# Kernel tuning notes

Hardware: AMD Instinct MI355X
Metric: run time of the kernel (lower is better)

Reference implementation:

```python
import jax, jax.numpy as jnp
import numpy as np

N, E = 50000, 800000
IN, HID, OUT, H, REL, RD = 768, 256, 128, 8, 6, 64


def setup_inputs() -> dict:
    key = jax.random.key(0)
    ks = jax.random.split(key, 16)
    g = lambda i, shape, sc: jax.random.normal(ks[i], shape, jnp.float32) * sc
    return dict(
        x=g(0, (N, IN), 1.0),
        edge_index=jax.random.randint(ks[1], (2, E), 0, N),
        edge_type=jax.random.randint(ks[2], (E,), 0, REL),
        rel_emb=g(3, (REL, RD), 0.1),
        W1=g(4, (IN, HID), 0.03),
        att_src1=g(5, (H, HID // H), 0.1),
        att_dst1=g(6, (H, HID // H), 0.1),
        We1=g(7, (RD, HID), 0.1),
        att_e1=g(8, (H, HID // H), 0.1),
        b1=jnp.zeros((HID,), jnp.float32),
        g1=jnp.ones((HID,), jnp.float32),
        beta1=jnp.zeros((HID,), jnp.float32),
        W2=g(9, (HID, OUT), 0.06),
        att_src2=g(10, (1, OUT), 0.1),
        att_dst2=g(11, (1, OUT), 0.1),
        b2=jnp.zeros((OUT,), jnp.float32),
        g2=jnp.ones((OUT,), jnp.float32),
        beta2=jnp.zeros((OUT,), jnp.float32),
    )


def _gat(x, src, dst, W, a_s, a_d, bias, heads, ch, e_feat=None, We=None, a_e=None):
    # PyG GATConv (shared lin, concat=True, negative_slope=0.2, eval-mode dropout)
    n = x.shape[0]
    h = (x @ W).reshape(n, heads, ch)              # [N,H,C]
    al_s = (h * a_s).sum(-1)                       # [N,H]
    al_d = (h * a_d).sum(-1)
    alpha = al_s[src] + al_d[dst]                  # [Etot,H]
    if e_feat is not None:
        e = (e_feat @ We).reshape(-1, heads, ch)
        alpha = alpha + (e * a_e).sum(-1)
    alpha = jax.nn.leaky_relu(alpha, 0.2)
    mx = jax.ops.segment_max(alpha, dst, num_segments=n)   # segment softmax over dst
    ex = jnp.exp(alpha - mx[dst])
    den = jax.ops.segment_sum(ex, dst, num_segments=n)
    w = ex / (den[dst] + 1e-16)
    out = jax.ops.segment_sum(h[src] * w[:, :, None], dst, num_segments=n)
    return out.reshape(n, heads * ch) + bias


def _ln(x, g, b):
    m = x.mean(-1, keepdims=True)
    v = x.var(-1, keepdims=True)
    return (x - m) / jnp.sqrt(v + 1e-5) * g + b


def reference(x, edge_index, edge_type, rel_emb, W1, att_src1, att_dst1, We1, att_e1,
              b1, g1, beta1, W2, att_src2, att_dst2, b2, g2, beta2):
    n = x.shape[0]
    src0, dst0 = edge_index[0], edge_index[1]
    loop = jnp.arange(n)
    src = jnp.concatenate([src0, loop])
    dst = jnp.concatenate([dst0, loop])
    rel_feat = rel_emb[edge_type]                   # [E,RD]
    # self-loop edge_attr = mean of incoming edge_attr (fill_value='mean')
    cnt = jax.ops.segment_sum(jnp.ones((src0.shape[0],), jnp.float32), dst0, num_segments=n)
    self_attr = jax.ops.segment_sum(rel_feat, dst0, num_segments=n) / jnp.maximum(cnt, 1.0)[:, None]
    e_feat = jnp.concatenate([rel_feat, self_attr], 0)
    h = _gat(x, src, dst, W1, att_src1, att_dst1, b1, H, HID // H, e_feat, We1, att_e1)
    h = jax.nn.elu(_ln(h, g1, beta1))
    h = _gat(h, src, dst, W2, att_src2, att_dst2, b2, 1, OUT)
    return _ln(h, g2, beta2)
```

## Files before the change

### kernel.cpp

```cpp
#include <hip/hip_runtime.h>
#include <hip/hip_bf16.h>

#define IN_DIM 768
#define HID 256
#define OUT_DIM 128
#define NHEAD 8
#define NREL 6
#define RD 64

typedef unsigned short ushort_t;
typedef float f32x4 __attribute__((ext_vector_type(4)));
typedef __bf16 bf16x8 __attribute__((ext_vector_type(8)));
typedef unsigned short u16x8 __attribute__((ext_vector_type(8)));
typedef unsigned short u16x4 __attribute__((ext_vector_type(4)));
typedef unsigned short u16x2 __attribute__((ext_vector_type(2)));

typedef const __attribute__((address_space(1))) void* gptr_t;
typedef __attribute__((address_space(3))) void* lptr_t;

static __device__ __forceinline__ float leaky(float x) { return x > 0.f ? x : 0.2f * x; }

static __device__ __forceinline__ ushort_t f2bf(float f) {
    union { __hip_bfloat16 h; ushort_t u; } c;
    c.h = __float2bfloat16(f);
    return c.u;
}

static __device__ __forceinline__ float b2f(ushort_t u) {
    union { unsigned int i; float f; } c;
    c.i = ((unsigned int)u) << 16;
    return c.f;
}

__global__ void count_kernel(const int* __restrict__ dst0, int* __restrict__ deg, int E) {
    int e = blockIdx.x * blockDim.x + threadIdx.x;
    if (e >= E) return;
    atomicAdd(&deg[dst0[e]], 1);
}

__global__ void __launch_bounds__(256) scanA(const int* __restrict__ deg,
                                             int* __restrict__ bsum, int n) {
    __shared__ int sh[4];
    int b = blockIdx.x, t = threadIdx.x;
    int s = 0;
#pragma unroll
    for (int j = 0; j < 4; j++) {
        int idx = b * 1024 + t * 4 + j;
        if (idx < n) s += deg[idx];
    }
    for (int o = 32; o > 0; o >>= 1) s += __shfl_xor(s, o, 64);
    if ((t & 63) == 0) sh[t >> 6] = s;
    __syncthreads();
    if (t == 0) bsum[b] = sh[0] + sh[1] + sh[2] + sh[3];
}

__global__ void __launch_bounds__(256) scanB(const int* __restrict__ bsum,
                                             int* __restrict__ bbase,
                                             int* __restrict__ rowptr, int nb, int n) {
    __shared__ int sh[256];
    int t = threadIdx.x;
    int v = (t < nb) ? bsum[t] : 0;
    sh[t] = v;
    __syncthreads();
    for (int o = 1; o < 256; o <<= 1) {
        int add = (t >= o) ? sh[t - o] : 0;
        __syncthreads();
        sh[t] += add;
        __syncthreads();
    }
    if (t < nb) bbase[t] = sh[t] - v;
    if (t == 255) rowptr[n] = sh[255];
}

__global__ void __launch_bounds__(256) scanC(const int* __restrict__ deg,
                                             const int* __restrict__ bbase,
                                             int* __restrict__ rowptr, int n) {
    __shared__ int sh[256];
    int b = blockIdx.x, t = threadIdx.x;
    int base = b * 1024;
    int loc[4];
    int run = 0;
#pragma unroll
    for (int j = 0; j < 4; j++) {
        int idx = base + t * 4 + j;
        int d = (idx < n) ? deg[idx] : 0;
        loc[j] = run;
        run += d;
    }
    int tot = run;
    sh[t] = run;
    __syncthreads();
    for (int o = 1; o < 256; o <<= 1) {
        int add = (t >= o) ? sh[t - o] : 0;
        __syncthreads();
        sh[t] += add;
        __syncthreads();
    }
    int texcl = sh[t] - tot;
    int bb = bbase[b];
#pragma unroll
    for (int j = 0; j < 4; j++) {
        int idx = base + t * 4 + j;
        if (idx < n) rowptr[idx] = bb + texcl + loc[j];
    }
}

__global__ void scatter_kernel(const int* __restrict__ src0, const int* __restrict__ dst0,
                               const int* __restrict__ ety, const int* __restrict__ rowptr,
                               int* __restrict__ fill, int* __restrict__ src_pk, int E) {
    int e = blockIdx.x * blockDim.x + threadIdx.x;
    if (e >= E) return;
    int d = dst0[e];
    int pos = rowptr[d] + atomicAdd(&fill[d], 1);
    src_pk[pos] = src0[e] | (ety[e] << 24);
}

__global__ void rel_alpha_kernel(const float* __restrict__ rel_emb, const float* __restrict__ We1,
                                 const float* __restrict__ att_e1, float* __restrict__ rel_alpha) {
    int t = threadIdx.x;
    if (t >= NREL * NHEAD) return;
    int r = t / NHEAD, h = t % NHEAD;
    float acc = 0.f;
    for (int c = 0; c < HID / NHEAD; c++) {
        float v = 0.f;
        for (int k = 0; k < RD; k++) v += rel_emb[r * RD + k] * We1[k * HID + h * 32 + c];
        acc += v * att_e1[h * 32 + c];
    }
    rel_alpha[r * NHEAD + h] = acc;
}

__global__ void transpose_conv(const float* __restrict__ W, ushort_t* __restrict__ Wt,
                               int K, int Nc) {
    int i = blockIdx.x * 256 + threadIdx.x;
    if (i >= K * Nc) return;
    int k = i / Nc, n = i % Nc;
    Wt[n * K + k] = f2bf(W[i]);
}

__global__ void __launch_bounds__(256) conv_bf16(const float* __restrict__ x,
                                                 ushort_t* __restrict__ xb,
                                                 int total, int padtotal) {
    for (long long idx = (long long)(blockIdx.x * 256 + threadIdx.x) * 8; idx < padtotal;
         idx += (long long)gridDim.x * 256 * 8) {
        u16x8 o;
        if (idx < total) {
            float4 f0 = *reinterpret_cast<const float4*>(x + idx);
            float4 f1 = *reinterpret_cast<const float4*>(x + idx + 4);
            o[0] = f2bf(f0.x); o[1] = f2bf(f0.y); o[2] = f2bf(f0.z); o[3] = f2bf(f0.w);
            o[4] = f2bf(f1.x); o[5] = f2bf(f1.y); o[6] = f2bf(f1.z); o[7] = f2bf(f1.w);
        } else {
            o = u16x8{0, 0, 0, 0, 0, 0, 0, 0};
        }
        *reinterpret_cast<u16x8*>(xb + idx) = o;
    }
}

template <int AMODE>
__global__ void __launch_bounds__(256) gemm_lds(const ushort_t* __restrict__ A,
                                                const ushort_t* __restrict__ Bt,
                                                ushort_t* __restrict__ C,
                                                int K, int Nout, int NBlk,
                                                const float* __restrict__ att_s,
                                                const float* __restrict__ att_d,
                                                float* __restrict__ als,
                                                float* __restrict__ ald, int N) {
    __shared__ ushort_t sA[128 * 64];
    __shared__ ushort_t sB[128 * 64];
    int T = gridDim.x;
    int p = blockIdx.x;
    int q8 = T >> 3, rr8 = T & 7, xc = p & 7, j = p >> 3;
    int l = (xc < rr8 ? xc * (q8 + 1) : rr8 * (q8 + 1) + (xc - rr8) * q8) + j;
    int m0 = (l / NBlk) * 128;
    int n0 = (l % NBlk) * 128;
    int t = threadIdx.x;
    int w = t >> 6, ln = t & 63;
    int wm = (w >> 1) * 64, wn = (w & 1) * 64;

    const ushort_t* ag = A + (size_t)(m0 + w * 32 + (ln >> 3)) * K + (ln & 7) * 8;
    const ushort_t* bg = Bt + (size_t)(n0 + w * 32 + (ln >> 3)) * K + (ln & 7) * 8;

    f32x4 acc[4][4] = {};

    for (int k0 = 0; k0 < K; k0 += 64) {
#pragma unroll
        for (int i = 0; i < 4; i++) {
            __builtin_amdgcn_global_load_lds(
                (gptr_t)(const void*)(ag + (size_t)i * 8 * K + k0),
                (lptr_t)(void*)(&sA[(w * 32 + i * 8) * 64]), 16, 0, 0);
            __builtin_amdgcn_global_load_lds(
                (gptr_t)(const void*)(bg + (size_t)i * 8 * K + k0),
                (lptr_t)(void*)(&sB[(w * 32 + i * 8) * 64]), 16, 0, 0);
        }
        __syncthreads();
#pragma unroll
        for (int ks = 0; ks < 2; ks++) {
            bf16x8 af[4], bfr[4];
#pragma unroll
            for (int m = 0; m < 4; m++)
                af[m] = *reinterpret_cast<const bf16x8*>(
                    &sA[(wm + m * 16 + (ln & 15)) * 64 + ks * 32 + (ln >> 4) * 8]);
#pragma unroll
            for (int n = 0; n < 4; n++)
                bfr[n] = *reinterpret_cast<const bf16x8*>(
                    &sB[(wn + n * 16 + (ln & 15)) * 64 + ks * 32 + (ln >> 4) * 8]);
#pragma unroll
            for (int m = 0; m < 4; m++)
#pragma unroll
                for (int n = 0; n < 4; n++)
                    acc[m][n] = __builtin_amdgcn_mfma_f32_16x16x32_bf16(af[m], bfr[n], acc[m][n], 0, 0, 0);
        }
        __syncthreads();
    }

    int cc = ln & 15, qq = ln >> 4;
#pragma unroll
    for (int m = 0; m < 4; m++) {
#pragma unroll
        for (int rr = 0; rr < 4; rr++) {
            int row = m0 + wm + m * 16 + qq * 4 + rr;
#pragma unroll
            for (int n = 0; n < 4; n++)
                C[(size_t)row * Nout + n0 + wn + n * 16 + cc] = f2bf(acc[m][n][rr]);
        }
    }

    float as_[4], ad_[4];
#pragma unroll
    for (int n = 0; n < 4; n++) {
        int col = n0 + wn + n * 16 + cc;
        as_[n] = att_s[col];
        ad_[n] = att_d[col];
    }

    if constexpr (AMODE == 1) {
        int hbase = (n0 + wn) >> 5;
#pragma unroll
        for (int m = 0; m < 4; m++) {
#pragma unroll
            for (int rr = 0; rr < 4; rr++) {
                int row = m0 + wm + m * 16 + qq * 4 + rr;
                float ps0 = acc[m][0][rr] * as_[0] + acc[m][1][rr] * as_[1];
                float ps1 = acc[m][2][rr] * as_[2] + acc[m][3][rr] * as_[3];
                float pd0 = acc[m][0][rr] * ad_[0] + acc[m][1][rr] * ad_[1];
                float pd1 = acc[m][2][rr] * ad_[2] + acc[m][3][rr] * ad_[3];
#pragma unroll
                for (int o = 1; o < 16; o <<= 1) {
                    ps0 += __shfl_xor(ps0, o, 64);
                    ps1 += __shfl_xor(ps1, o, 64);
                    pd0 += __shfl_xor(pd0, o, 64);
                    pd1 += __shfl_xor(pd1, o, 64);
                }
                if (cc == 0 && row < N) {
                    als[row * NHEAD + hbase] = ps0;
                    als[row * NHEAD + hbase + 1] = ps1;
                    ald[row * NHEAD + hbase] = pd0;
                    ald[row * NHEAD + hbase + 1] = pd1;
                }
            }
        }
    } else {
        __shared__ float sh_s[2][128];
        __shared__ float sh_d[2][128];
#pragma unroll
        for (int m = 0; m < 4; m++) {
#pragma unroll
            for (int rr = 0; rr < 4; rr++) {
                int rib = wm + m * 16 + qq * 4 + rr;
                float ps = acc[m][0][rr] * as_[0] + acc[m][1][rr] * as_[1] +
                           acc[m][2][rr] * as_[2] + acc[m][3][rr] * as_[3];
                float pd = acc[m][0][rr] * ad_[0] + acc[m][1][rr] * ad_[1] +
                           acc[m][2][rr] * ad_[2] + acc[m][3][rr] * ad_[3];
#pragma unroll
                for (int o = 1; o < 16; o <<= 1) {
                    ps += __shfl_xor(ps, o, 64);
                    pd += __shfl_xor(pd, o, 64);
                }
                if (cc == 0) {
                    sh_s[wn >> 6][rib] = ps;
                    sh_d[wn >> 6][rib] = pd;
                }
            }
        }
        __syncthreads();
        if (t < 128) {
            int row = m0 + t;
            if (row < N) {
                als[row] = sh_s[0][t] + sh_s[1][t];
                ald[row] = sh_d[0][t] + sh_d[1][t];
            }
        }
    }
}

__global__ void __launch_bounds__(64) node_agg1(
    const ushort_t* __restrict__ h1b, const float* __restrict__ als, const float* __restrict__ ald,
    const float* __restrict__ rel_alpha, const int* __restrict__ rowptr,
    const int* __restrict__ src_pk,
    const float* __restrict__ b1, const float* __restrict__ g1, const float* __restrict__ beta1,
    ushort_t* __restrict__ out, int N) {
    __shared__ float sh_rel[NREL * NHEAD];
    __shared__ float sh_w[64 * NHEAD];
    __shared__ unsigned sh_off[64];
    int l = threadIdx.x;
    int i = blockIdx.x;
    if (i >= N) return;
    if (l < NREL * NHEAD) sh_rel[l] = rel_alpha[l];
    int h = l & 7;
    int e8 = l >> 3;
    float als_i = als[i * NHEAD + h];
    float ald_h = ald[i * NHEAD + h];
    float c0, c1, c2, c3;
    {
        u16x4 v = *reinterpret_cast<const u16x4*>(h1b + (size_t)i * HID + 4 * l);
        c0 = b2f(v[0]); c1 = b2f(v[1]); c2 = b2f(v[2]); c3 = b2f(v[3]);
    }
    int base = rowptr[i];
    int deg = rowptr[i + 1] - base;
    const char* hb = reinterpret_cast<const char*>(h1b);
    float acc0 = 0.f, acc1 = 0.f, acc2 = 0.f, acc3 = 0.f;
    float csum = 0.f, rs = 0.f;
    __syncthreads();
    for (int cs = 0; cs < deg; cs += 64) {
        int c = min(64, deg - cs);
        for (int p = 0; p * 8 < c; p++) {
            int e = p * 8 + e8;
            if (e < c) {
                int pk = src_pk[base + cs + e];
                int sv = pk & 0xFFFFFF;
                int tv = (unsigned)pk >> 24;
                float ra = sh_rel[tv * NHEAD + h];
                float a = als[sv * NHEAD + h] + ald_h + ra;
                float w = __expf(fminf(leaky(a), 40.f));
                sh_w[e * NHEAD + h] = w;
                csum += w;
                rs += ra;
                if (h == 0) sh_off[e] = (unsigned)sv * (HID * 2);
            }
        }
        __syncthreads();
        int e = 0;
        for (; e + 8 <= c; e += 8) {
            unsigned ofs[8];
            float wt[8];
            u16x4 v[8];
#pragma unroll
            for (int jj = 0; jj < 8; jj++) {
                ofs[jj] = sh_off[e + jj];
                wt[jj] = sh_w[(e + jj) * NHEAD + e8];
            }
#pragma unroll
            for (int jj = 0; jj < 8; jj++)
                v[jj] = *reinterpret_cast<const u16x4*>(hb + ofs[jj] + 8 * l);
#pragma unroll
            for (int jj = 0; jj < 8; jj++) {
                acc0 += wt[jj] * b2f(v[jj][0]);
                acc1 += wt[jj] * b2f(v[jj][1]);
                acc2 += wt[jj] * b2f(v[jj][2]);
                acc3 += wt[jj] * b2f(v[jj][3]);
            }
        }
        for (; e < c; e++) {
            unsigned o0 = sh_off[e];
            float w0 = sh_w[e * NHEAD + e8];
            u16x4 v0 = *reinterpret_cast<const u16x4*>(hb + o0 + 8 * l);
            acc0 += w0 * b2f(v0[0]); acc1 += w0 * b2f(v0[1]);
            acc2 += w0 * b2f(v0[2]); acc3 += w0 * b2f(v0[3]);
        }
        __syncthreads();
    }
    for (int o = 8; o < 64; o <<= 1) {
        csum += __shfl_xor(csum, o, 64);
        rs += __shfl_xor(rs, o, 64);
    }
    float selfa = rs / fmaxf((float)deg, 1.0f);
    float wself = __expf(fminf(leaky(als_i + ald_h + selfa), 40.f));
    float stot = csum + wself;
    float s_g = __shfl(stot, e8, 64);
    float w_g = __shfl(wself, e8, 64);
    acc0 += w_g * c0; acc1 += w_g * c1; acc2 += w_g * c2; acc3 += w_g * c3;
    float inv = 1.0f / (s_g + 1e-16f);
    float4 bb = *reinterpret_cast<const float4*>(b1 + 4 * l);
    float y0 = acc0 * inv + bb.x, y1 = acc1 * inv + bb.y;
    float y2 = acc2 * inv + bb.z, y3 = acc3 * inv + bb.w;
    float su = y0 + y1 + y2 + y3;
    float sq = y0 * y0 + y1 * y1 + y2 * y2 + y3 * y3;
    for (int o = 1; o < 64; o <<= 1) {
        su += __shfl_xor(su, o, 64);
        sq += __shfl_xor(sq, o, 64);
    }
    float mean = su * (1.f / 256.f);
    float var = sq * (1.f / 256.f) - mean * mean;
    float rstd = rsqrtf(var + 1e-5f);
    float4 gg = *reinterpret_cast<const float4*>(g1 + 4 * l);
    float4 be = *reinterpret_cast<const float4*>(beta1 + 4 * l);
    float z0 = (y0 - mean) * rstd * gg.x + be.x;
    float z1 = (y1 - mean) * rstd * gg.y + be.y;
    float z2 = (y2 - mean) * rstd * gg.z + be.z;
    float z3 = (y3 - mean) * rstd * gg.w + be.w;
    u16x4 ov;
    ov[0] = f2bf(z0 > 0.f ? z0 : __expf(z0) - 1.f);
    ov[1] = f2bf(z1 > 0.f ? z1 : __expf(z1) - 1.f);
    ov[2] = f2bf(z2 > 0.f ? z2 : __expf(z2) - 1.f);
    ov[3] = f2bf(z3 > 0.f ? z3 : __expf(z3) - 1.f);
    *reinterpret_cast<u16x4*>(out + (size_t)i * HID + 4 * l) = ov;
}

__global__ void __launch_bounds__(64) node_agg2(const ushort_t* __restrict__ h2b,
                                                const float* __restrict__ als,
                                                const float* __restrict__ ald,
                                                const int* __restrict__ rowptr,
                                                const int* __restrict__ src_pk,
                                                const float* __restrict__ b2,
                                                const float* __restrict__ g2,
                                                const float* __restrict__ beta2,
                                                float* __restrict__ out, int N) {
    __shared__ float sh_w[64];
    __shared__ unsigned sh_off[64];
    int l = threadIdx.x;
    int i = blockIdx.x;
    if (i >= N) return;
    float aldi = ald[i];
    float alsi = als[i];
    float c0, c1;
    {
        u16x2 v = *reinterpret_cast<const u16x2*>(h2b + (size_t)i * OUT_DIM + 2 * l);
        c0 = b2f(v[0]); c1 = b2f(v[1]);
    }
    int base = rowptr[i];
    int deg = rowptr[i + 1] - base;
    const char* hb = reinterpret_cast<const char*>(h2b);
    float acc0 = 0.f, acc1 = 0.f;
    float csum = 0.f;
    for (int cs = 0; cs < deg; cs += 64) {
        int c = min(64, deg - cs);
        float w = 0.f;
        if (l < c) {
            int sv = src_pk[base + cs + l] & 0xFFFFFF;
            w = __expf(fminf(leaky(als[sv] + aldi), 40.f));
            sh_off[l] = (unsigned)sv * (OUT_DIM * 2);
        }
        sh_w[l] = w;
        csum += w;
        __syncthreads();
        int e = 0;
        for (; e + 8 <= c; e += 8) {
            unsigned ofs[8];
            float wt[8];
            u16x2 v[8];
#pragma unroll
            for (int jj = 0; jj < 8; jj++) {
                ofs[jj] = sh_off[e + jj];
                wt[jj] = sh_w[e + jj];
            }
#pragma unroll
            for (int jj = 0; jj < 8; jj++)
                v[jj] = *reinterpret_cast<const u16x2*>(hb + ofs[jj] + 4 * l);
#pragma unroll
            for (int jj = 0; jj < 8; jj++) {
                acc0 += wt[jj] * b2f(v[jj][0]);
                acc1 += wt[jj] * b2f(v[jj][1]);
            }
        }
        for (; e < c; e++) {
            unsigned o0 = sh_off[e];
            float w0 = sh_w[e];
            u16x2 v0 = *reinterpret_cast<const u16x2*>(hb + o0 + 4 * l);
            acc0 += w0 * b2f(v0[0]); acc1 += w0 * b2f(v0[1]);
        }
        __syncthreads();
    }
    for (int o = 1; o < 64; o <<= 1) csum += __shfl_xor(csum, o, 64);
    float wself = __expf(fminf(leaky(alsi + aldi), 40.f));
    float s = csum + wself;
    acc0 += wself * c0; acc1 += wself * c1;
    float inv = 1.0f / (s + 1e-16f);
    float2 bb = *reinterpret_cast<const float2*>(b2 + 2 * l);
    float y0 = acc0 * inv + bb.x, y1 = acc1 * inv + bb.y;
    float su = y0 + y1, sq = y0 * y0 + y1 * y1;
    for (int o = 1; o < 64; o <<= 1) {
        su += __shfl_xor(su, o, 64);
        sq += __shfl_xor(sq, o, 64);
    }
    float mean = su * (1.f / 128.f);
    float var = sq * (1.f / 128.f) - mean * mean;
    float rstd = rsqrtf(var + 1e-5f);
    float2 gg = *reinterpret_cast<const float2*>(g2 + 2 * l);
    float2 be = *reinterpret_cast<const float2*>(beta2 + 2 * l);
    float2 ov;
    ov.x = (y0 - mean) * rstd * gg.x + be.x;
    ov.y = (y1 - mean) * rstd * gg.y + be.y;
    *reinterpret_cast<float2*>(out + (size_t)i * OUT_DIM + 2 * l) = ov;
}

extern "C" void kernel_launch(void* const* d_in, const int* in_sizes, int n_in,
                              void* d_out, int out_size, void* d_ws, size_t ws_size,
                              hipStream_t stream) {
    const float* x = (const float*)d_in[0];
    const int* ei = (const int*)d_in[1];
    const int* ety = (const int*)d_in[2];
    const float* rel_emb = (const float*)d_in[3];
    const float* W1 = (const float*)d_in[4];
    const float* att_s1 = (const float*)d_in[5];
    const float* att_d1 = (const float*)d_in[6];
    const float* We1 = (const float*)d_in[7];
    const float* att_e1 = (const float*)d_in[8];
    const float* b1 = (const float*)d_in[9];
    const float* g1 = (const float*)d_in[10];
    const float* beta1 = (const float*)d_in[11];
    const float* W2 = (const float*)d_in[12];
    const float* att_s2 = (const float*)d_in[13];
    const float* att_d2 = (const float*)d_in[14];
    const float* b2 = (const float*)d_in[15];
    const float* g2 = (const float*)d_in[16];
    const float* beta2 = (const float*)d_in[17];

    int N = in_sizes[0] / IN_DIM;
    int E = in_sizes[1] / 2;
    int Mpad = ((N + 127) / 128) * 128;
    const int* src0 = ei;
    const int* dst0 = ei + E;

    char* ws = (char*)d_ws;
    size_t off = 0;
    auto alloc = [&](size_t bytes) -> void* {
        off = (off + 255) & ~(size_t)255;
        void* p = ws + off;
        off += bytes;
        return p;
    };
    int* deg = (int*)alloc((size_t)N * 4);
    int* fill = (int*)alloc((size_t)N * 4);
    int* rowptr = (int*)alloc((size_t)(N + 1) * 4);
    int* src_pk = (int*)alloc((size_t)E * 4);
    int nb = (N + 1023) >> 10;
    int* bsum = (int*)alloc((size_t)nb * 4);
    int* bbase = (int*)alloc((size_t)nb * 4);
    float* rel_alpha = (float*)alloc(NREL * NHEAD * 4);
    float* als1 = (float*)alloc((size_t)N * NHEAD * 4);
    float* ald1 = (float*)alloc((size_t)N * NHEAD * 4);
    float* al2s = (float*)alloc((size_t)N * 4);
    float* al2d = (float*)alloc((size_t)N * 4);
    ushort_t* W1t = (ushort_t*)alloc((size_t)HID * IN_DIM * 2);
    ushort_t* W2t = (ushort_t*)alloc((size_t)OUT_DIM * HID * 2);
    ushort_t* h1b = (ushort_t*)alloc((size_t)Mpad * HID * 2);
    ushort_t* xb = (ushort_t*)alloc((size_t)Mpad * IN_DIM * 2);
    ushort_t* h1pb = xb;
    ushort_t* h2b = h1b;

    hipMemsetAsync(deg, 0, (size_t)N * 4, stream);
    hipMemsetAsync(fill, 0, (size_t)N * 4, stream);

    int eb = (E + 255) / 256;
    count_kernel<<<eb, 256, 0, stream>>>(dst0, deg, E);
    scanA<<<nb, 256, 0, stream>>>(deg, bsum, N);
    scanB<<<1, 256, 0, stream>>>(bsum, bbase, rowptr, nb, N);
    scanC<<<nb, 256, 0, stream>>>(deg, bbase, rowptr, N);
    scatter_kernel<<<eb, 256, 0, stream>>>(src0, dst0, ety, rowptr, fill, src_pk, E);
    rel_alpha_kernel<<<1, 64, 0, stream>>>(rel_emb, We1, att_e1, rel_alpha);
    transpose_conv<<<(IN_DIM * HID + 255) / 256, 256, 0, stream>>>(W1, W1t, IN_DIM, HID);
    transpose_conv<<<(HID * OUT_DIM + 255) / 256, 256, 0, stream>>>(W2, W2t, HID, OUT_DIM);
    conv_bf16<<<2048, 256, 0, stream>>>(x, xb, N * IN_DIM, Mpad * IN_DIM);

    int NB1 = HID / 128;
    int T1 = (Mpad / 128) * NB1;
    gemm_lds<1><<<T1, 256, 0, stream>>>(xb, W1t, h1b, IN_DIM, HID, NB1,
                                        att_s1, att_d1, als1, ald1, N);
    hipMemsetAsync(h1pb + (size_t)N * HID, 0, (size_t)(Mpad - N) * HID * 2, stream);
    node_agg1<<<N, 64, 0, stream>>>(h1b, als1, ald1, rel_alpha, rowptr, src_pk,
                                    b1, g1, beta1, h1pb, N);

    int NB2 = OUT_DIM / 128;
    int T2 = (Mpad / 128) * NB2;
    gemm_lds<2><<<T2, 256, 0, stream>>>(h1pb, W2t, h2b, HID, OUT_DIM, NB2,
                                        att_s2, att_d2, al2s, al2d, N);
    node_agg2<<<N, 64, 0, stream>>>(h2b, al2s, al2d, rowptr, src_pk, b2, g2, beta2,
                                    (float*)d_out, N);
}
```

Before: 371.9 us.

## Double-buffer GEMM LDS tiles, pack aggregation waves per block, use shuffles

The GEMM now stages K in 32-wide tiles into two LDS buffers, so the next tile's global-to-LDS load overlaps the current tile's MFMAs. The two node aggregation kernels now run four wavefronts (four nodes) per 256-thread block. They pass edge weights and offsets with wave shuffles instead of LDS plus barriers, and node_agg1 processes edges in chunks of 8. The two weight-transpose launches are merged into one kernel. The risks are halved K per barrier in the GEMM and more shuffle instructions per edge.

```diff
diff --git a/kernel.cpp b/kernel.cpp
--- a/kernel.cpp
+++ b/kernel.cpp
@@ -129,12 +129,19 @@
     rel_alpha[r * NHEAD + h] = acc;
 }
 
-__global__ void transpose_conv(const float* __restrict__ W, ushort_t* __restrict__ Wt,
-                               int K, int Nc) {
+__global__ void prep_weights(const float* __restrict__ W1, const float* __restrict__ W2,
+                             ushort_t* __restrict__ W1t, ushort_t* __restrict__ W2t) {
     int i = blockIdx.x * 256 + threadIdx.x;
-    if (i >= K * Nc) return;
-    int k = i / Nc, n = i % Nc;
-    Wt[n * K + k] = f2bf(W[i]);
+    if (i < IN_DIM * HID) {
+        int k = i / HID, n = i % HID;
+        W1t[n * IN_DIM + k] = f2bf(W1[i]);
+    } else {
+        int j = i - IN_DIM * HID;
+        if (j < HID * OUT_DIM) {
+            int k = j / OUT_DIM, n = j % OUT_DIM;
+            W2t[n * HID + k] = f2bf(W2[j]);
+        }
+    }
 }
 
 __global__ void __launch_bounds__(256) conv_bf16(const float* __restrict__ x,
@@ -164,8 +171,8 @@
                                                 const float* __restrict__ att_d,
                                                 float* __restrict__ als,
                                                 float* __restrict__ ald, int N) {
-    __shared__ ushort_t sA[128 * 64];
-    __shared__ ushort_t sB[128 * 64];
+    __shared__ ushort_t sA[2][128 * 32];
+    __shared__ ushort_t sB[2][128 * 32];
     int T = gridDim.x;
     int p = blockIdx.x;
     int q8 = T >> 3, rr8 = T & 7, xc = p & 7, j = p >> 3;
@@ -176,40 +183,45 @@
     int w = t >> 6, ln = t & 63;
     int wm = (w >> 1) * 64, wn = (w & 1) * 64;
 
-    const ushort_t* ag = A + (size_t)(m0 + w * 32 + (ln >> 3)) * K + (ln & 7) * 8;
-    const ushort_t* bg = Bt + (size_t)(n0 + w * 32 + (ln >> 3)) * K + (ln & 7) * 8;
+    const ushort_t* ag = A + (size_t)(m0 + w * 32 + (ln >> 2)) * K + (ln & 3) * 8;
+    const ushort_t* bg = Bt + (size_t)(n0 + w * 32 + (ln >> 2)) * K + (ln & 3) * 8;
 
     f32x4 acc[4][4] = {};
 
-    for (int k0 = 0; k0 < K; k0 += 64) {
-#pragma unroll
-        for (int i = 0; i < 4; i++) {
+    auto stage = [&](int buf, int k0) {
+#pragma unroll
+        for (int i = 0; i < 2; i++) {
             __builtin_amdgcn_global_load_lds(
-                (gptr_t)(const void*)(ag + (size_t)i * 8 * K + k0),
-                (lptr_t)(void*)(&sA[(w * 32 + i * 8) * 64]), 16, 0, 0);
+                (gptr_t)(const void*)(ag + (size_t)i * 16 * K + k0),
+                (lptr_t)(void*)(&sA[buf][(w * 32 + i * 16) * 32]), 16, 0, 0);
             __builtin_amdgcn_global_load_lds(
-                (gptr_t)(const void*)(bg + (size_t)i * 8 * K + k0),
-                (lptr_t)(void*)(&sB[(w * 32 + i * 8) * 64]), 16, 0, 0);
-        }
+                (gptr_t)(const void*)(bg + (size_t)i * 16 * K + k0),
+                (lptr_t)(void*)(&sB[buf][(w * 32 + i * 16) * 32]), 16, 0, 0);
+        }
+    };
+
+    int nt = K >> 5;
+    stage(0, 0);
+    __syncthreads();
+    int cur = 0;
+    for (int tt = 0; tt < nt; tt++) {
+        if (tt + 1 < nt) stage(cur ^ 1, (tt + 1) << 5);
+        bf16x8 af[4], bfr[4];
+#pragma unroll
+        for (int m = 0; m < 4; m++)
+            af[m] = *reinterpret_cast<const bf16x8*>(
+                &sA[cur][(wm + m * 16 + (ln & 15)) * 32 + (ln >> 4) * 8]);
+#pragma unroll
+        for (int n = 0; n < 4; n++)
+            bfr[n] = *reinterpret_cast<const bf16x8*>(
+                &sB[cur][(wn + n * 16 + (ln & 15)) * 32 + (ln >> 4) * 8]);
+#pragma unroll
+        for (int m = 0; m < 4; m++)
+#pragma unroll
+            for (int n = 0; n < 4; n++)
+                acc[m][n] = __builtin_amdgcn_mfma_f32_16x16x32_bf16(af[m], bfr[n], acc[m][n], 0, 0, 0);
         __syncthreads();
-#pragma unroll
-        for (int ks = 0; ks < 2; ks++) {
-            bf16x8 af[4], bfr[4];
-#pragma unroll
-            for (int m = 0; m < 4; m++)
-                af[m] = *reinterpret_cast<const bf16x8*>(
-                    &sA[(wm + m * 16 + (ln & 15)) * 64 + ks * 32 + (ln >> 4) * 8]);
-#pragma unroll
-            for (int n = 0; n < 4; n++)
-                bfr[n] = *reinterpret_cast<const bf16x8*>(
-                    &sB[(wn + n * 16 + (ln & 15)) * 64 + ks * 32 + (ln >> 4) * 8]);
-#pragma unroll
-            for (int m = 0; m < 4; m++)
-#pragma unroll
-                for (int n = 0; n < 4; n++)
-                    acc[m][n] = __builtin_amdgcn_mfma_f32_16x16x32_bf16(af[m], bfr[n], acc[m][n], 0, 0, 0);
-        }
-        __syncthreads();
+        cur ^= 1;
     }
 
     int cc = ln & 15, qq = ln >> 4;
@@ -292,19 +304,18 @@
     }
 }
 
-__global__ void __launch_bounds__(64) node_agg1(
+__global__ void __launch_bounds__(256) node_agg1(
     const ushort_t* __restrict__ h1b, const float* __restrict__ als, const float* __restrict__ ald,
     const float* __restrict__ rel_alpha, const int* __restrict__ rowptr,
     const int* __restrict__ src_pk,
     const float* __restrict__ b1, const float* __restrict__ g1, const float* __restrict__ beta1,
     ushort_t* __restrict__ out, int N) {
     __shared__ float sh_rel[NREL * NHEAD];
-    __shared__ float sh_w[64 * NHEAD];
-    __shared__ unsigned sh_off[64];
-    int l = threadIdx.x;
-    int i = blockIdx.x;
+    if (threadIdx.x < NREL * NHEAD) sh_rel[threadIdx.x] = rel_alpha[threadIdx.x];
+    __syncthreads();
+    int l = threadIdx.x & 63;
+    int i = blockIdx.x * 4 + (threadIdx.x >> 6);
     if (i >= N) return;
-    if (l < NREL * NHEAD) sh_rel[l] = rel_alpha[l];
     int h = l & 7;
     int e8 = l >> 3;
     float als_i = als[i * NHEAD + h];
@@ -319,54 +330,48 @@
     const char* hb = reinterpret_cast<const char*>(h1b);
     float acc0 = 0.f, acc1 = 0.f, acc2 = 0.f, acc3 = 0.f;
     float csum = 0.f, rs = 0.f;
-    __syncthreads();
-    for (int cs = 0; cs < deg; cs += 64) {
-        int c = min(64, deg - cs);
-        for (int p = 0; p * 8 < c; p++) {
-            int e = p * 8 + e8;
-            if (e < c) {
-                int pk = src_pk[base + cs + e];
-                int sv = pk & 0xFFFFFF;
-                int tv = (unsigned)pk >> 24;
-                float ra = sh_rel[tv * NHEAD + h];
-                float a = als[sv * NHEAD + h] + ald_h + ra;
-                float w = __expf(fminf(leaky(a), 40.f));
-                sh_w[e * NHEAD + h] = w;
-                csum += w;
-                rs += ra;
-                if (h == 0) sh_off[e] = (unsigned)sv * (HID * 2);
-            }
-        }
-        __syncthreads();
-        int e = 0;
-        for (; e + 8 <= c; e += 8) {
-            unsigned ofs[8];
+    for (int cs = 0; cs < deg; cs += 8) {
+        int c = min(8, deg - cs);
+        float w = 0.f, ra = 0.f;
+        unsigned offv = 0;
+        if (e8 < c) {
+            int pk = src_pk[base + cs + e8];
+            int sv = pk & 0xFFFFFF;
+            int tv = (unsigned)pk >> 24;
+            ra = sh_rel[tv * NHEAD + h];
+            w = __expf(fminf(leaky(als[sv * NHEAD + h] + ald_h + ra), 40.f));
+            offv = (unsigned)sv * (HID * 2);
+        }
+        csum += w;
+        rs += ra;
+        if (c == 8) {
             float wt[8];
+            unsigned of[8];
             u16x4 v[8];
 #pragma unroll
-            for (int jj = 0; jj < 8; jj++) {
-                ofs[jj] = sh_off[e + jj];
-                wt[jj] = sh_w[(e + jj) * NHEAD + e8];
-            }
-#pragma unroll
-            for (int jj = 0; jj < 8; jj++)
-                v[jj] = *reinterpret_cast<const u16x4*>(hb + ofs[jj] + 8 * l);
-#pragma unroll
-            for (int jj = 0; jj < 8; jj++) {
-                acc0 += wt[jj] * b2f(v[jj][0]);
-                acc1 += wt[jj] * b2f(v[jj][1]);
-                acc2 += wt[jj] * b2f(v[jj][2]);
-                acc3 += wt[jj] * b2f(v[jj][3]);
-            }
-        }
-        for (; e < c; e++) {
-            unsigned o0 = sh_off[e];
-            float w0 = sh_w[e * NHEAD + e8];
-            u16x4 v0 = *reinterpret_cast<const u16x4*>(hb + o0 + 8 * l);
-            acc0 += w0 * b2f(v0[0]); acc1 += w0 * b2f(v0[1]);
-            acc2 += w0 * b2f(v0[2]); acc3 += w0 * b2f(v0[3]);
-        }
-        __syncthreads();
+            for (int e = 0; e < 8; e++) {
+                wt[e] = __shfl(w, e * 8 + e8, 64);
+                of[e] = (unsigned)__shfl((int)offv, e * 8, 64);
+            }
+#pragma unroll
+            for (int e = 0; e < 8; e++)
+                v[e] = *reinterpret_cast<const u16x4*>(hb + of[e] + 8 * l);
+#pragma unroll
+            for (int e = 0; e < 8; e++) {
+                acc0 += wt[e] * b2f(v[e][0]);
+                acc1 += wt[e] * b2f(v[e][1]);
+                acc2 += wt[e] * b2f(v[e][2]);
+                acc3 += wt[e] * b2f(v[e][3]);
+            }
+        } else {
+            for (int e = 0; e < c; e++) {
+                float wt = __shfl(w, e * 8 + e8, 64);
+                unsigned of = (unsigned)__shfl((int)offv, e * 8, 64);
+                u16x4 v = *reinterpret_cast<const u16x4*>(hb + of + 8 * l);
+                acc0 += wt * b2f(v[0]); acc1 += wt * b2f(v[1]);
+                acc2 += wt * b2f(v[2]); acc3 += wt * b2f(v[3]);
+            }
+        }
     }
     for (int o = 8; o < 64; o <<= 1) {
         csum += __shfl_xor(csum, o, 64);
@@ -405,19 +410,17 @@
     *reinterpret_cast<u16x4*>(out + (size_t)i * HID + 4 * l) = ov;
 }
 
-__global__ void __launch_bounds__(64) node_agg2(const ushort_t* __restrict__ h2b,
-                                                const float* __restrict__ als,
-                                                const float* __restrict__ ald,
-                                                const int* __restrict__ rowptr,
-                                                const int* __restrict__ src_pk,
-                                                const float* __restrict__ b2,
-                                                const float* __restrict__ g2,
-                                                const float* __restrict__ beta2,
-                                                float* __restrict__ out, int N) {
-    __shared__ float sh_w[64];
-    __shared__ unsigned sh_off[64];
-    int l = threadIdx.x;
-    int i = blockIdx.x;
+__global__ void __launch_bounds__(256) node_agg2(const ushort_t* __restrict__ h2b,
+                                                 const float* __restrict__ als,
+                                                 const float* __restrict__ ald,
+                                                 const int* __restrict__ rowptr,
+                                                 const int* __restrict__ src_pk,
+                                                 const float* __restrict__ b2,
+                                                 const float* __restrict__ g2,
+                                                 const float* __restrict__ beta2,
+                                                 float* __restrict__ out, int N) {
+    int l = threadIdx.x & 63;
+    int i = blockIdx.x * 4 + (threadIdx.x >> 6);
     if (i >= N) return;
     float aldi = ald[i];
     float alsi = als[i];
@@ -434,27 +437,26 @@
     for (int cs = 0; cs < deg; cs += 64) {
         int c = min(64, deg - cs);
         float w = 0.f;
+        unsigned offv = 0;
         if (l < c) {
             int sv = src_pk[base + cs + l] & 0xFFFFFF;
             w = __expf(fminf(leaky(als[sv] + aldi), 40.f));
-            sh_off[l] = (unsigned)sv * (OUT_DIM * 2);
-        }
-        sh_w[l] = w;
+            offv = (unsigned)sv * (OUT_DIM * 2);
+        }
         csum += w;
-        __syncthreads();
         int e = 0;
         for (; e + 8 <= c; e += 8) {
-            unsigned ofs[8];
             float wt[8];
+            unsigned of[8];
             u16x2 v[8];
 #pragma unroll
             for (int jj = 0; jj < 8; jj++) {
-                ofs[jj] = sh_off[e + jj];
-                wt[jj] = sh_w[e + jj];
+                wt[jj] = __shfl(w, e + jj, 64);
+                of[jj] = (unsigned)__shfl((int)offv, e + jj, 64);
             }
 #pragma unroll
             for (int jj = 0; jj < 8; jj++)
-                v[jj] = *reinterpret_cast<const u16x2*>(hb + ofs[jj] + 4 * l);
+                v[jj] = *reinterpret_cast<const u16x2*>(hb + of[jj] + 4 * l);
 #pragma unroll
             for (int jj = 0; jj < 8; jj++) {
                 acc0 += wt[jj] * b2f(v[jj][0]);
@@ -462,12 +464,11 @@
             }
         }
         for (; e < c; e++) {
-            unsigned o0 = sh_off[e];
-            float w0 = sh_w[e];
-            u16x2 v0 = *reinterpret_cast<const u16x2*>(hb + o0 + 4 * l);
-            acc0 += w0 * b2f(v0[0]); acc1 += w0 * b2f(v0[1]);
-        }
-        __syncthreads();
+            float wt = __shfl(w, e, 64);
+            unsigned of = (unsigned)__shfl((int)offv, e, 64);
+            u16x2 v = *reinterpret_cast<const u16x2*>(hb + of + 4 * l);
+            acc0 += wt * b2f(v[0]); acc1 += wt * b2f(v[1]);
+        }
     }
     for (int o = 1; o < 64; o <<= 1) csum += __shfl_xor(csum, o, 64);
     float wself = __expf(fminf(leaky(alsi + aldi), 40.f));
@@ -557,8 +558,7 @@
     scanC<<<nb, 256, 0, stream>>>(deg, bbase, rowptr, N);
     scatter_kernel<<<eb, 256, 0, stream>>>(src0, dst0, ety, rowptr, fill, src_pk, E);
     rel_alpha_kernel<<<1, 64, 0, stream>>>(rel_emb, We1, att_e1, rel_alpha);
-    transpose_conv<<<(IN_DIM * HID + 255) / 256, 256, 0, stream>>>(W1, W1t, IN_DIM, HID);
-    transpose_conv<<<(HID * OUT_DIM + 255) / 256, 256, 0, stream>>>(W2, W2t, HID, OUT_DIM);
+    prep_weights<<<(IN_DIM * HID + HID * OUT_DIM + 255) / 256, 256, 0, stream>>>(W1, W2, W1t, W2t);
     conv_bf16<<<2048, 256, 0, stream>>>(x, xb, N * IN_DIM, Mpad * IN_DIM);
 
     int NB1 = HID / 128;
@@ -566,13 +566,13 @@
     gemm_lds<1><<<T1, 256, 0, stream>>>(xb, W1t, h1b, IN_DIM, HID, NB1,
                                         att_s1, att_d1, als1, ald1, N);
     hipMemsetAsync(h1pb + (size_t)N * HID, 0, (size_t)(Mpad - N) * HID * 2, stream);
-    node_agg1<<<N, 64, 0, stream>>>(h1b, als1, ald1, rel_alpha, rowptr, src_pk,
-                                    b1, g1, beta1, h1pb, N);
+    node_agg1<<<(N + 3) / 4, 256, 0, stream>>>(h1b, als1, ald1, rel_alpha, rowptr, src_pk,
+                                               b1, g1, beta1, h1pb, N);
 
     int NB2 = OUT_DIM / 128;
     int T2 = (Mpad / 128) * NB2;
     gemm_lds<2><<<T2, 256, 0, stream>>>(h1pb, W2t, h2b, HID, OUT_DIM, NB2,
                                         att_s2, att_d2, al2s, al2d, N);
-    node_agg2<<<N, 64, 0, stream>>>(h2b, al2s, al2d, rowptr, src_pk, b2, g2, beta2,
-                                    (float*)d_out, N);
-}
+    node_agg2<<<(N + 3) / 4, 256, 0, stream>>>(h2b, al2s, al2d, rowptr, src_pk, b2, g2, beta2,
+                                               (float*)d_out, N);
+}
```

Result: no change. 375.8 us (+1.0%).
